# Kernel optimization log

Hardware: AMD Instinct MI355X
Metric: run time of the kernel (lower is better)

The kernel has to match this reference:

```python
import jax, jax.numpy as jnp
import numpy as np

B_SZ = 64
SEQ = 2048
IN_DIM = 16
D_MODEL = 128
D_INNER = 256   # expand(2) * d_model
D_STATE = 16
N_LAYERS = 5
N_PARAMS = 3
IDX_PRICE, IDX_RY, IDX_GY, IDX_NY = 0, 1, 2, 3


def setup_inputs() -> dict:
    key = jax.random.key(0)
    ks = iter(jax.random.split(key, 64))
    def nrm(shape, scale=0.02):
        return jax.random.normal(next(ks), shape, jnp.float32) * scale
    inp = {}
    # forward args
    inp["origins"] = jax.random.uniform(next(ks), (B_SZ, SEQ, IN_DIM), jnp.float32, 0.5, 1.5)
    inp["x"] = jax.random.normal(next(ks), (B_SZ, SEQ, IN_DIM), jnp.float32)
    # input embedding
    inp["emb_w"] = nrm((IN_DIM, D_MODEL)); inp["emb_b"] = jnp.zeros((D_MODEL,), jnp.float32)
    # per-layer Mamba block params, stacked on leading n_layers dim
    inp["in_w"] = nrm((N_LAYERS, D_MODEL, 2 * D_INNER)); inp["in_b"] = jnp.zeros((N_LAYERS, 2 * D_INNER), jnp.float32)
    inp["xp_w"] = nrm((N_LAYERS, D_INNER, 2 * D_STATE)); inp["xp_b"] = jnp.zeros((N_LAYERS, 2 * D_STATE), jnp.float32)
    inp["dt_w"] = nrm((N_LAYERS, D_INNER, D_INNER));     inp["dt_b"] = jnp.zeros((N_LAYERS, D_INNER), jnp.float32)
    inp["out_w"] = nrm((N_LAYERS, D_INNER, D_MODEL));    inp["out_b"] = jnp.zeros((N_LAYERS, D_MODEL), jnp.float32)
    # A_log init: log(arange(1, d_state+1)) broadcast over d_inner
    a = jnp.log(jnp.arange(1, D_STATE + 1, dtype=jnp.float32))
    inp["A_log"] = jnp.broadcast_to(a, (N_LAYERS, D_INNER, D_STATE)).copy()
    inp["Dp"] = jnp.ones((N_LAYERS, D_INNER), jnp.float32)
    # layernorms
    inp["ln_g"] = jnp.ones((N_LAYERS, D_MODEL), jnp.float32)
    inp["ln_b"] = jnp.zeros((N_LAYERS, D_MODEL), jnp.float32)
    # output head: Linear(128,64) -> ReLU -> Linear(64,3) -> Sigmoid
    inp["o1_w"] = nrm((D_MODEL, D_MODEL // 2)); inp["o1_b"] = jnp.zeros((D_MODEL // 2,), jnp.float32)
    inp["o2_w"] = nrm((D_MODEL // 2, N_PARAMS)); inp["o2_b"] = jnp.zeros((N_PARAMS,), jnp.float32)
    return inp


def _silu(x):
    return x * jax.nn.sigmoid(x)


def _layernorm(x, g, b, eps=1e-5):
    mu = jnp.mean(x, axis=-1, keepdims=True)
    var = jnp.mean(jnp.square(x - mu), axis=-1, keepdims=True)
    return (x - mu) * jax.lax.rsqrt(var + eps) * g + b


def _mamba_block(x, iw, ib, xw, xb, dw, db, ow, ob, alog, d):
    # x: [B, S, D_MODEL]
    xz = x @ iw + ib                       # [B,S,2*di]
    x_proj, z = jnp.split(xz, 2, axis=-1)  # [B,S,di] each
    u = _silu(x_proj)                      # no conv path (use_conv=False)
    A = -jnp.exp(alog)                     # [di, ds]
    x_dbl = u @ xw + xb                    # [B,S,2*ds]
    Bm, Cm = jnp.split(x_dbl, 2, axis=-1)  # [B,S,ds]
    dt = jax.nn.softplus(u @ dw + db)      # [B,S,di]

    def step(h, t):
        u_t, dt_t, B_t, C_t = t            # [B,di],[B,di],[B,ds],[B,ds]
        dA = jnp.exp(dt_t[:, :, None] * A)                 # [B,di,ds]
        h = h * dA + (dt_t * u_t)[:, :, None] * B_t[:, None, :]
        y = jnp.sum(h * C_t[:, None, :], axis=-1) + d * u_t  # [B,di]
        return h, y

    h0 = jnp.zeros((u.shape[0], u.shape[2], A.shape[-1]), u.dtype)
    xs = (jnp.swapaxes(u, 0, 1), jnp.swapaxes(dt, 0, 1),
          jnp.swapaxes(Bm, 0, 1), jnp.swapaxes(Cm, 0, 1))  # seq-major
    _, ys = jax.lax.scan(step, h0, xs)     # ys: [S,B,di]
    y = jnp.swapaxes(ys, 0, 1)             # [B,S,di]
    y = y * _silu(z)
    return y @ ow + ob                     # [B,S,D_MODEL]


def _forward(origins, x, emb_w, emb_b, in_w, in_b, xp_w, xp_b, dt_w, dt_b,
             out_w, out_b, A_log, Dp, ln_g, ln_b, o1_w, o1_b, o2_w, o2_b):
    h = x @ emb_w + emb_b
    for l in range(N_LAYERS):
        res = h
        h = _mamba_block(h, in_w[l], in_b[l], xp_w[l], xp_b[l], dt_w[l], dt_b[l],
                         out_w[l], out_b[l], A_log[l], Dp[l])
        h = _layernorm(h + res, ln_g[l], ln_b[l])
    pooled = jnp.mean(h, axis=1)                         # lengths=None path
    hid = jax.nn.relu(pooled @ o1_w + o1_b)              # dropout is eval no-op
    params = jax.nn.sigmoid(hid @ o2_w + o2_b) * 2.0     # [B, 3]
    a, b, c = params[:, 0], params[:, 1], params[:, 2]
    last_1 = origins[:, -1, :]
    last_2 = origins[:, -2, :]
    price = last_1[:, IDX_PRICE]
    ry_now, ry_before = last_1[:, IDX_RY], last_2[:, IDX_RY]
    gy_now, gy_before = last_1[:, IDX_GY], last_2[:, IDX_GY]
    ny_now, ny_before = last_1[:, IDX_NY], last_2[:, IDX_NY]
    out = price * a * ry_now / ry_before * 2.0 * (
        b * jax.nn.sigmoid(gy_now - gy_before) + c * jax.nn.sigmoid(ny_now - ny_before))
    return out  # [B]


def reference(origins, x, emb_w, emb_b, in_w, in_b, xp_w, xp_b, dt_w, dt_b,
              out_w, out_b, A_log, Dp, ln_g, ln_b, o1_w, o1_b, o2_w, o2_b):
    return _forward(origins, x, emb_w, emb_b, in_w, in_b, xp_w, xp_b, dt_w, dt_b,
                    out_w, out_b, A_log, Dp, ln_g, ln_b, o1_w, o1_b, o2_w, o2_b)
```

## Files before the change

### kernel.cpp

```cpp
#include <hip/hip_runtime.h>
#include <hip/hip_bf16.h>
#include <math.h>

#define B_SZ    64
#define SEQ     2048
#define DMODEL  128
#define DINNER  256
#define DSTATE  16
#define NLAYERS 5

typedef unsigned short u16;
typedef __attribute__((ext_vector_type(8))) short bf16x8;
typedef __attribute__((ext_vector_type(4))) float f32x4;

static __device__ __forceinline__ float bf2f(u16 u){
  union { unsigned u; float f; } a; a.u = ((unsigned)u) << 16; return a.f;
}
static __device__ __forceinline__ u16 f2bf(float f){
  union { float f; unsigned u; } a; a.f = f;
  unsigned r = a.u + 0x7fffu + ((a.u >> 16) & 1u);
  return (u16)(r >> 16);
}
static __device__ __forceinline__ float sigm(float x){ return 1.f/(1.f+__expf(-x)); }
static __device__ __forceinline__ float siluf(float x){ return x/(1.f+__expf(-x)); }

#define MFMA16(a,b,c) __builtin_amdgcn_mfma_f32_16x16x32_bf16((a),(b),(c),0,0,0)

__global__ __launch_bounds__(256) void prep_kernel(
    const float* __restrict__ in_w, const float* __restrict__ xp_w,
    const float* __restrict__ dt_w, const float* __restrict__ out_w,
    u16* __restrict__ WT1, u16* __restrict__ WT2, u16* __restrict__ WT3){
  int idx = blockIdx.x*256 + threadIdx.x;
  const int n1 = NLAYERS*512*128, n2 = NLAYERS*288*256, n3 = NLAYERS*128*256;
  if (idx < n1){
    int l = idx/(512*128), r = idx%(512*128), n = r/128, k = r%128;
    WT1[idx] = f2bf(in_w[((size_t)l*128 + k)*512 + n]);
  } else if (idx < n1+n2){
    int t = idx-n1; int l=t/(288*256), r=t%(288*256), n=r/256, k=r%256;
    float v = (n<32) ? xp_w[((size_t)l*256+k)*32 + n]
                     : dt_w[((size_t)l*256+k)*256 + (n-32)];
    WT2[t] = f2bf(v);
  } else if (idx < n1+n2+n3){
    int t = idx-n1-n2; int l=t/(128*256), r=t%(128*256), n=r/256, k=r%256;
    WT3[t] = f2bf(out_w[((size_t)l*256+k)*128 + n]);
  }
}

__global__ __launch_bounds__(256) void emb_kernel(
    const float* __restrict__ x, const float* __restrict__ ew,
    const float* __restrict__ eb, u16* __restrict__ Hb, size_t cs){
  int idx = blockIdx.x*256 + threadIdx.x;
  int m = idx >> 7, d = idx & 127;
  float s = eb[d];
  #pragma unroll
  for (int k=0;k<16;++k) s += x[(size_t)m*16+k]*ew[k*128+d];
  Hb[(size_t)(d>>4)*cs + (size_t)m*16 + (d&15)] = f2bf(s);
}

__global__ __launch_bounds__(256) void gemm1_kernel(
    const u16* __restrict__ Hb, const u16* __restrict__ WT,
    const float* __restrict__ bias, u16* __restrict__ U, u16* __restrict__ ZS,
    size_t cs){
  const int lane = threadIdx.x & 63, wave = threadIdx.x >> 6;
  const int half = blockIdx.x & 1;
  const int m0 = (blockIdx.x >> 1)*256 + wave*64;
  const int lr = lane & 15, kg = lane >> 4;
  bf16x8 hfrag[4][4];
  #pragma unroll
  for (int g=0; g<4; ++g)
    #pragma unroll
    for (int f=0; f<4; ++f)
      hfrag[g][f] = *(const bf16x8*)(Hb + (size_t)((kg>>1)+2*f)*cs
                                     + (size_t)(m0+g*16+lr)*16 + (kg&1)*8);
  u16* const dst = half ? ZS : U;
  const u16* wrow = WT + (size_t)(half*256+lr)*128 + kg*8;
  bf16x8 wv[4];
  #pragma unroll
  for (int f=0; f<4; ++f) wv[f] = *(const bf16x8*)(wrow + f*32);
  #pragma unroll
  for (int nn=0; nn<16; ++nn){
    bf16x8 wn[4];
    if (nn < 15){
      const u16* wr2 = wrow + (size_t)(nn+1)*16*128;
      #pragma unroll
      for (int f=0; f<4; ++f) wn[f] = *(const bf16x8*)(wr2 + f*32);
    }
    f32x4 acc[4];
    #pragma unroll
    for (int g=0; g<4; ++g){
      acc[g] = (f32x4){0.f,0.f,0.f,0.f};
      #pragma unroll
      for (int f=0; f<4; ++f) acc[g] = MFMA16(wv[f], hfrag[g][f], acc[g]);
    }
    float4 bs4 = *(const float4*)(bias + half*256 + nn*16 + kg*4);
    #pragma unroll
    for (int g=0; g<4; ++g){
      ushort4 uv;
      uv.x = f2bf(siluf(acc[g][0]+bs4.x));
      uv.y = f2bf(siluf(acc[g][1]+bs4.y));
      uv.z = f2bf(siluf(acc[g][2]+bs4.z));
      uv.w = f2bf(siluf(acc[g][3]+bs4.w));
      *(ushort4*)(dst + (size_t)nn*cs + (size_t)(m0+g*16+lr)*16 + kg*4) = uv;
    }
    #pragma unroll
    for (int f=0; f<4; ++f) wv[f] = wn[f];
  }
}

template<int BF>
__global__ __launch_bounds__(256) void gemm2_kernel(
    const u16* __restrict__ Uin, const u16* __restrict__ WT,
    const float* __restrict__ xpb, const float* __restrict__ dtb,
    void* __restrict__ BCv, u16* __restrict__ DT, size_t cs){
  const int lane = threadIdx.x & 63, wave = threadIdx.x >> 6;
  const int m0 = blockIdx.x*128 + wave*32;
  const int lr = lane & 15, kg = lane >> 4;
  bf16x8 hfrag[2][8];
  #pragma unroll
  for (int g=0; g<2; ++g)
    #pragma unroll
    for (int f=0; f<8; ++f)
      hfrag[g][f] = *(const bf16x8*)(Uin + (size_t)((kg>>1)+2*f)*cs
                                     + (size_t)(m0+g*16+lr)*16 + (kg&1)*8);
  const u16* wrow = WT + (size_t)lr*256 + kg*8;
  bf16x8 wv[8];
  #pragma unroll
  for (int f=0; f<8; ++f) wv[f] = *(const bf16x8*)(wrow + f*32);
  #pragma unroll
  for (int nn=0; nn<18; ++nn){
    bf16x8 wn[8];
    if (nn < 17){
      const u16* wr2 = wrow + (size_t)(nn+1)*16*256;
      #pragma unroll
      for (int f=0; f<8; ++f) wn[f] = *(const bf16x8*)(wr2 + f*32);
    }
    f32x4 acc[2];
    #pragma unroll
    for (int g=0; g<2; ++g){
      acc[g] = (f32x4){0.f,0.f,0.f,0.f};
      #pragma unroll
      for (int f=0; f<8; ++f) acc[g] = MFMA16(wv[f], hfrag[g][f], acc[g]);
    }
    const int col0 = nn*16 + kg*4;
    if (col0 < 32){
      float4 bs4 = *(const float4*)(xpb + col0);
      #pragma unroll
      for (int g=0; g<2; ++g){
        if (BF){
          float4 ov;
          ov.x = acc[g][0]+bs4.x; ov.y = acc[g][1]+bs4.y;
          ov.z = acc[g][2]+bs4.z; ov.w = acc[g][3]+bs4.w;
          *(float4*)((float*)BCv + (size_t)nn*cs + (size_t)(m0+g*16+lr)*16 + kg*4) = ov;
        } else {
          ushort4 uv;
          uv.x = f2bf(acc[g][0]+bs4.x); uv.y = f2bf(acc[g][1]+bs4.y);
          uv.z = f2bf(acc[g][2]+bs4.z); uv.w = f2bf(acc[g][3]+bs4.w);
          *(ushort4*)((u16*)BCv + (size_t)nn*cs + (size_t)(m0+g*16+lr)*16 + kg*4) = uv;
        }
      }
    } else {
      float4 bs4 = *(const float4*)(dtb + (col0-32));
      #pragma unroll
      for (int g=0; g<2; ++g){
        float v0=acc[g][0]+bs4.x, v1=acc[g][1]+bs4.y;
        float v2=acc[g][2]+bs4.z, v3=acc[g][3]+bs4.w;
        ushort4 uv;
        uv.x = f2bf(fmaxf(v0,0.f) + __logf(1.f + __expf(-fabsf(v0))));
        uv.y = f2bf(fmaxf(v1,0.f) + __logf(1.f + __expf(-fabsf(v1))));
        uv.z = f2bf(fmaxf(v2,0.f) + __logf(1.f + __expf(-fabsf(v2))));
        uv.w = f2bf(fmaxf(v3,0.f) + __logf(1.f + __expf(-fabsf(v3))));
        *(ushort4*)(DT + (size_t)(nn-2)*cs + (size_t)(m0+g*16+lr)*16 + kg*4) = uv;
      }
    }
    #pragma unroll
    for (int f=0; f<8; ++f) wv[f] = wn[f];
  }
}

static __device__ __forceinline__ void powtree(float r, float* pw){
  float p2=r*r, p3=p2*r, p4=p2*p2;
  float p5=p4*r, p6=p4*p2, p7=p4*p3, p8=p4*p4;
  pw[0]=r;  pw[1]=p2; pw[2]=p3; pw[3]=p4;
  pw[4]=p5; pw[5]=p6; pw[6]=p7; pw[7]=p8;
  pw[8]=p8*r;  pw[9]=p8*p2;  pw[10]=p8*p3;  pw[11]=p8*p4;
  pw[12]=p8*p5; pw[13]=p8*p6; pw[14]=p8*p7; pw[15]=p8*p8;
}


template<int BF>
__global__ __launch_bounds__(256) void scan_p1(
    const u16* __restrict__ U, const u16* __restrict__ DT,
    const void* __restrict__ BCv, const float* __restrict__ Alog,
    u16* __restrict__ SGH, size_t cs, int nseg, int L){
  const int seg = blockIdx.x % nseg;
  const int b   = blockIdx.x / nseg;
  const int c   = threadIdx.x;
  const size_t coff = (size_t)(c>>4)*cs + (c&15);
  float a2[16]; bool geo = true;
  #pragma unroll
  for (int i=0;i<16;++i){
    float A = -__expf(Alog[c*16+i]);
    a2[i] = A * 1.44269504f;
    if (fabsf(A + (float)(i+1)) > 1e-3f) geo = false;
  }
  float h[16];
  #pragma unroll
  for (int i=0;i<16;++i) h[i]=0.f;
  float sdt = 0.f;
  const size_t mbase = (size_t)b*SEQ + (size_t)seg*L;
  if (geo){
    #pragma unroll 2
    for (int t=0;t<L;++t){
      const size_t m = mbase + t;
      float u  = bf2f(U [coff + m*16]);
      float dt = bf2f(DT[coff + m*16]);
      float Bv[16];
      if (BF){
        const float* bp = (const float*)BCv + m*16;
        #pragma unroll
        for (int i=0;i<16;++i) Bv[i] = bp[i];
      } else {
        bf16x8 b0 = *(const bf16x8*)((const u16*)BCv + m*16);
        bf16x8 b1 = *(const bf16x8*)((const u16*)BCv + m*16 + 8);
        #pragma unroll
        for (int i=0;i<8;++i){ Bv[i]=bf2f((u16)b0[i]); Bv[i+8]=bf2f((u16)b1[i]); }
      }
      float du = dt*u; sdt += dt;
      float r = exp2f(-1.44269504f*dt);
      float pw[16]; powtree(r, pw);
      #pragma unroll
      for (int i=0;i<16;++i) h[i] = h[i]*pw[i] + du*Bv[i];
    }
  } else {
    for (int t=0;t<L;++t){
      const size_t m = mbase + t;
      float u  = bf2f(U [coff + m*16]);
      float dt = bf2f(DT[coff + m*16]);
      float Bv[16];
      if (BF){
        const float* bp = (const float*)BCv + m*16;
        #pragma unroll
        for (int i=0;i<16;++i) Bv[i] = bp[i];
      } else {
        bf16x8 b0 = *(const bf16x8*)((const u16*)BCv + m*16);
        bf16x8 b1 = *(const bf16x8*)((const u16*)BCv + m*16 + 8);
        #pragma unroll
        for (int i=0;i<8;++i){ Bv[i]=bf2f((u16)b0[i]); Bv[i+8]=bf2f((u16)b1[i]); }
      }
      float du = dt*u; sdt += dt;
      #pragma unroll
      for (int i=0;i<16;++i)
        h[i] = h[i]*exp2f(dt*a2[i]) + du*Bv[i];
    }
  }
  const size_t kb = ((size_t)b*nseg+seg);
  #pragma unroll
  for (int i=0;i<16;++i) SGH[(kb*17+i)*256 + c] = f2bf(h[i]);
  SGH[(kb*17+16)*256 + c] = f2bf(sdt);
}

__global__ __launch_bounds__(256) void scan_p2(
    u16* __restrict__ SGH, const float* __restrict__ Alog, int nseg){
  const int i = blockIdx.x & 15, b = blockIdx.x >> 4, c = threadIdx.x;
  const float a2 = -__expf(Alog[c*16+i]) * 1.44269504f;
  float h = 0.f;
  for (int s=0;s<nseg;++s){
    const size_t kb = ((size_t)b*nseg+s);
    float sdt = bf2f(SGH[(kb*17+16)*256 + c]);
    size_t k = (kb*17+i)*256 + c;
    float hl = bf2f(SGH[k]);
    SGH[k] = f2bf(h);
    h = h*exp2f(sdt*a2) + hl;
  }
}

template<int BF>
__global__ __launch_bounds__(256) void scan_p3(
    u16* __restrict__ UY, const u16* __restrict__ DT, const void* __restrict__ BCv,
    const u16* __restrict__ ZS, const float* __restrict__ Alog,
    const float* __restrict__ Dp, const u16* __restrict__ SGH, size_t cs,
    int nseg, int L){
  const int seg = blockIdx.x % nseg;
  const int b   = blockIdx.x / nseg;
  const int c   = threadIdx.x;
  const size_t coff = (size_t)(c>>4)*cs + (c&15);
  float a2[16]; bool geo = true;
  #pragma unroll
  for (int i=0;i<16;++i){
    float A = -__expf(Alog[c*16+i]);
    a2[i] = A * 1.44269504f;
    if (fabsf(A + (float)(i+1)) > 1e-3f) geo = false;
  }
  const float Dv = Dp[c];
  const size_t kb = ((size_t)b*nseg+seg);
  float h[16];
  #pragma unroll
  for (int i=0;i<16;++i) h[i] = bf2f(SGH[(kb*17+i)*256 + c]);
  const size_t mbase = (size_t)b*SEQ + (size_t)seg*L;
  if (geo){
    #pragma unroll 2
    for (int t=0;t<L;++t){
      const size_t m = mbase + t;
      float u  = bf2f(UY[coff + m*16]);
      float dt = bf2f(DT[coff + m*16]);
      float zs = bf2f(ZS[coff + m*16]);
      float Bv[16], Cv[16];
      if (BF){
        const float* bp = (const float*)BCv + m*16;
        const float* cp = (const float*)BCv + cs + m*16;
        #pragma unroll
        for (int i=0;i<16;++i){ Bv[i]=bp[i]; Cv[i]=cp[i]; }
      } else {
        const u16* bc = (const u16*)BCv;
        bf16x8 b0 = *(const bf16x8*)(bc + m*16);
        bf16x8 b1 = *(const bf16x8*)(bc + m*16 + 8);
        bf16x8 c0 = *(const bf16x8*)(bc + cs + m*16);
        bf16x8 c1 = *(const bf16x8*)(bc + cs + m*16 + 8);
        #pragma unroll
        for (int i=0;i<8;++i){
          Bv[i]=bf2f((u16)b0[i]); Bv[i+8]=bf2f((u16)b1[i]);
          Cv[i]=bf2f((u16)c0[i]); Cv[i+8]=bf2f((u16)c1[i]);
        }
      }
      float du = dt*u;
      float r = exp2f(-1.44269504f*dt);
      float pw[16]; powtree(r, pw);
      float s0=0.f, s1=0.f;
      #pragma unroll
      for (int i=0;i<8;++i){
        h[i] = h[i]*pw[i] + du*Bv[i];
        s0 += h[i]*Cv[i];
      }
      #pragma unroll
      for (int i=8;i<16;++i){
        h[i] = h[i]*pw[i] + du*Bv[i];
        s1 += h[i]*Cv[i];
      }
      float y = s0 + s1 + Dv*u;
      UY[coff + m*16] = f2bf(y*zs);
    }
  } else {
    for (int t=0;t<L;++t){
      const size_t m = mbase + t;
      float u  = bf2f(UY[coff + m*16]);
      float dt = bf2f(DT[coff + m*16]);
      float zs = bf2f(ZS[coff + m*16]);
      float Bv[16], Cv[16];
      if (BF){
        const float* bp = (const float*)BCv + m*16;
        const float* cp = (const float*)BCv + cs + m*16;
        #pragma unroll
        for (int i=0;i<16;++i){ Bv[i]=bp[i]; Cv[i]=cp[i]; }
      } else {
        const u16* bc = (const u16*)BCv;
        bf16x8 b0 = *(const bf16x8*)(bc + m*16);
        bf16x8 b1 = *(const bf16x8*)(bc + m*16 + 8);
        bf16x8 c0 = *(const bf16x8*)(bc + cs + m*16);
        bf16x8 c1 = *(const bf16x8*)(bc + cs + m*16 + 8);
        #pragma unroll
        for (int i=0;i<8;++i){
          Bv[i]=bf2f((u16)b0[i]); Bv[i+8]=bf2f((u16)b1[i]);
          Cv[i]=bf2f((u16)c0[i]); Cv[i+8]=bf2f((u16)c1[i]);
        }
      }
      float du = dt*u;
      float s0=0.f;
      #pragma unroll
      for (int i=0;i<16;++i){
        h[i] = h[i]*exp2f(dt*a2[i]) + du*Bv[i];
        s0 += h[i]*Cv[i];
      }
      float y = s0 + Dv*u;
      UY[coff + m*16] = f2bf(y*zs);
    }
  }
}

__global__ __launch_bounds__(256) void gemm3ln_kernel(
    const u16* __restrict__ YS, const u16* __restrict__ WT,
    const float* __restrict__ ob, const float* __restrict__ g,
    const float* __restrict__ bb, u16* __restrict__ Hb, size_t cs){
  const int lane = threadIdx.x & 63, wave = threadIdx.x >> 6;
  const int m0 = blockIdx.x*128 + wave*32;
  const int lr = lane & 15, kg = lane >> 4;
  bf16x8 hfrag[2][8];
  #pragma unroll
  for (int gg=0; gg<2; ++gg)
    #pragma unroll
    for (int f=0; f<8; ++f)
      hfrag[gg][f] = *(const bf16x8*)(YS + (size_t)((kg>>1)+2*f)*cs
                                      + (size_t)(m0+gg*16+lr)*16 + (kg&1)*8);
  const u16* wrow = WT + (size_t)lr*256 + kg*8;
  bf16x8 wv[8];
  #pragma unroll
  for (int f=0; f<8; ++f) wv[f] = *(const bf16x8*)(wrow + f*32);
  ushort4 xvp[2][8];
  float s[2] = {0.f,0.f}, q[2] = {0.f,0.f};
  #pragma unroll
  for (int n=0; n<8; ++n){
    bf16x8 wn[8];
    if (n < 7){
      const u16* wr2 = wrow + (size_t)(n+1)*16*256;
      #pragma unroll
      for (int f=0; f<8; ++f) wn[f] = *(const bf16x8*)(wr2 + f*32);
    }
    float4 bs4 = *(const float4*)(ob + n*16 + kg*4);
    #pragma unroll
    for (int gg=0; gg<2; ++gg){
      f32x4 acc = {0.f,0.f,0.f,0.f};
      #pragma unroll
      for (int f=0; f<8; ++f) acc = MFMA16(wv[f], hfrag[gg][f], acc);
      const size_t m = (size_t)(m0 + gg*16 + lr);
      ushort4 rs = *(const ushort4*)(Hb + (size_t)n*cs + m*16 + kg*4);
      float x0 = acc[0] + bs4.x + bf2f(rs.x);
      float x1 = acc[1] + bs4.y + bf2f(rs.y);
      float x2 = acc[2] + bs4.z + bf2f(rs.z);
      float x3 = acc[3] + bs4.w + bf2f(rs.w);
      s[gg] += (x0+x1)+(x2+x3);
      q[gg] += (x0*x0+x1*x1)+(x2*x2+x3*x3);
      ushort4 pv; pv.x=f2bf(x0); pv.y=f2bf(x1); pv.z=f2bf(x2); pv.w=f2bf(x3);
      xvp[gg][n] = pv;
    }
    #pragma unroll
    for (int f=0; f<8; ++f) wv[f] = wn[f];
  }
  #pragma unroll
  for (int gg=0; gg<2; ++gg){
    float ss = s[gg], qq = q[gg];
    ss += __shfl_xor(ss,16); qq += __shfl_xor(qq,16);
    ss += __shfl_xor(ss,32); qq += __shfl_xor(qq,32);
    float mu  = ss * 0.0078125f;
    float var = qq * 0.0078125f - mu*mu;
    float inv = rsqrtf(var + 1e-5f);
    const size_t m = (size_t)(m0 + gg*16 + lr);
    #pragma unroll
    for (int n=0;n<8;++n){
      float4 g4 = *(const float4*)(g  + n*16 + kg*4);
      float4 b4 = *(const float4*)(bb + n*16 + kg*4);
      ushort4 pv = xvp[gg][n];
      ushort4 uv;
      uv.x = f2bf((bf2f(pv.x)-mu)*inv*g4.x + b4.x);
      uv.y = f2bf((bf2f(pv.y)-mu)*inv*g4.y + b4.y);
      uv.z = f2bf((bf2f(pv.z)-mu)*inv*g4.z + b4.z);
      uv.w = f2bf((bf2f(pv.w)-mu)*inv*g4.w + b4.w);
      *(ushort4*)(Hb + (size_t)n*cs + m*16 + kg*4) = uv;
    }
  }
}

__global__ __launch_bounds__(128) void pool1_kernel(
    const u16* __restrict__ Hb, float* __restrict__ PP, size_t cs){
  const int blk = blockIdx.x;
  const int tc = blk & 15, b = blk >> 4;
  const int d = threadIdx.x;
  const size_t coff = (size_t)(d>>4)*cs + (d&15);
  float s = 0.f;
  const size_t base = ((size_t)b*SEQ + tc*128);
  for (int t=0;t<128;++t) s += bf2f(Hb[coff + (base+t)*16]);
  PP[((size_t)b*16 + tc)*128 + d] = s;
}
__global__ __launch_bounds__(128) void pool2_kernel(
    const float* __restrict__ PP, float* __restrict__ P){
  const int b = blockIdx.x, d = threadIdx.x;
  float s = 0.f;
  #pragma unroll
  for (int tc=0;tc<16;++tc) s += PP[((size_t)b*16+tc)*128 + d];
  P[b*128 + d] = s * (1.f/SEQ);
}

__global__ __launch_bounds__(64) void head_kernel(
    const float* __restrict__ P, const float* __restrict__ o1w,
    const float* __restrict__ o1b, const float* __restrict__ o2w,
    const float* __restrict__ o2b, const float* __restrict__ origins,
    float* __restrict__ out){
  const int b = blockIdx.x;
  const int j = threadIdx.x;
  float hv = o1b[j];
  #pragma unroll 4
  for (int d=0; d<128; ++d) hv += P[b*128+d]*o1w[d*64+j];
  hv = fmaxf(hv, 0.f);
  float p0 = hv*o2w[j*3+0], p1 = hv*o2w[j*3+1], p2 = hv*o2w[j*3+2];
  #pragma unroll
  for (int o=1;o<64;o<<=1){
    p0 += __shfl_xor(p0,o); p1 += __shfl_xor(p1,o); p2 += __shfl_xor(p2,o);
  }
  if (j == 0){
    float a = 2.f*sigm(p0 + o2b[0]);
    float bb = 2.f*sigm(p1 + o2b[1]);
    float c = 2.f*sigm(p2 + o2b[2]);
    const float* l1 = origins + ((size_t)b*SEQ + (SEQ-1))*16;
    const float* l2 = origins + ((size_t)b*SEQ + (SEQ-2))*16;
    float price=l1[0], ry_n=l1[1], ry_b=l2[1], gy_n=l1[2], gy_b=l2[2], ny_n=l1[3], ny_b=l2[3];
    out[b] = price*a*ry_n/ry_b*2.f*(bb*sigm(gy_n-gy_b) + c*sigm(ny_n-ny_b));
  }
}

extern "C" void kernel_launch(void* const* d_in, const int* in_sizes, int n_in,
                              void* d_out, int out_size, void* d_ws, size_t ws_size,
                              hipStream_t stream){
  const float* origins = (const float*)d_in[0];
  const float* x      = (const float*)d_in[1];
  const float* emb_w  = (const float*)d_in[2];
  const float* emb_b  = (const float*)d_in[3];
  const float* in_w   = (const float*)d_in[4];
  const float* in_b   = (const float*)d_in[5];
  const float* xp_w   = (const float*)d_in[6];
  const float* xp_b   = (const float*)d_in[7];
  const float* dt_w   = (const float*)d_in[8];
  const float* dt_b   = (const float*)d_in[9];
  const float* out_w  = (const float*)d_in[10];
  const float* out_b  = (const float*)d_in[11];
  const float* A_log  = (const float*)d_in[12];
  const float* Dp     = (const float*)d_in[13];
  const float* ln_g   = (const float*)d_in[14];
  const float* ln_b   = (const float*)d_in[15];
  const float* o1_w   = (const float*)d_in[16];
  const float* o1_b   = (const float*)d_in[17];
  const float* o2_w   = (const float*)d_in[18];
  const float* o2_b   = (const float*)d_in[19];
  float* outp = (float*)d_out;

  auto al = [](size_t b)->size_t{ return (b + 255) & ~(size_t)255; };
  const size_t wt1_b = al((size_t)NLAYERS*512*128*2);
  const size_t wt2_b = al((size_t)NLAYERS*288*256*2);
  const size_t wt3_b = al((size_t)NLAYERS*128*256*2);
  const size_t po_b  = al((size_t)B_SZ*128*4);
  const size_t pp_b  = al((size_t)B_SZ*16*128*4);
  const size_t fixed = wt1_b + wt2_b + wt3_b + po_b;

  int CB = 0, NSEG = 0, BCF = 0;
  size_t hb_b=0, u_b=0, bc_b=0, sg_b=0;
  static const int cbc[7]  = {64,32,16,8,4,2,1};
  static const int nsc[4]  = {32,16,32,16};
  static const int bfc[4]  = {1,1,0,0};
  for (int i=0;i<7 && !CB;++i){
    int cb = cbc[i];
    size_t csz = (size_t)cb*SEQ*16;
    for (int k=0;k<4;++k){
      int ns = nsc[k], bf = bfc[k];
      size_t hbb = al(8*csz*2);
      size_t uu  = al(16*csz*2);
      size_t bb  = al(2*csz*(bf?4:2));
      size_t sg  = al((size_t)cb*ns*17*256*2);
      size_t ov  = (sg > pp_b) ? sg : pp_b;
      if (fixed + hbb + 3*uu + bb + ov <= ws_size){
        CB=cb; NSEG=ns; BCF=bf; hb_b=hbb; u_b=uu; bc_b=bb; sg_b=ov; break;
      }
    }
  }
  if (!CB) return;

  char* ws = (char*)d_ws;
  size_t off = 0;
  auto take = [&](size_t bytes)->char*{ char* p = ws + off; off += bytes; return p; };
  u16*   WT1 = (u16*)take(wt1_b);
  u16*   WT2 = (u16*)take(wt2_b);
  u16*   WT3 = (u16*)take(wt3_b);
  float* PO  = (float*)take(po_b);
  u16*   Hb  = (u16*)take(hb_b);
  u16*   U   = (u16*)take(u_b);
  u16*   ZS  = (u16*)take(u_b);
  u16*   DT  = (u16*)take(u_b);
  void*  BC  = (void*)take(bc_b);
  u16*   SGH = (u16*)take(sg_b);
  float* PP  = (float*)SGH;

  prep_kernel<<<3360, 256, 0, stream>>>(in_w, xp_w, dt_w, out_w, WT1, WT2, WT3);

  const int NC = B_SZ / CB;
  const int Mc = CB * SEQ;
  const int L  = SEQ / NSEG;
  const size_t cs = (size_t)Mc*16;
  for (int ci=0; ci<NC; ++ci){
    const int b0 = ci * CB;
    const size_t R0 = (size_t)b0 * SEQ;
    emb_kernel<<<(Mc*DMODEL)/256, 256, 0, stream>>>(x + R0*16, emb_w, emb_b, Hb, cs);
    for (int l=0;l<NLAYERS;++l){
      const float* Al = A_log + (size_t)l*DINNER*DSTATE;
      gemm1_kernel<<<(Mc/256)*2, 256, 0, stream>>>(Hb, WT1 + (size_t)l*512*128,
                                                   in_b + l*512, U, ZS, cs);
      if (BCF)
        gemm2_kernel<1><<<Mc/128, 256, 0, stream>>>(U, WT2 + (size_t)l*288*256,
                                                    xp_b + l*32, dt_b + l*256, BC, DT, cs);
      else
        gemm2_kernel<0><<<Mc/128, 256, 0, stream>>>(U, WT2 + (size_t)l*288*256,
                                                    xp_b + l*32, dt_b + l*256, BC, DT, cs);
      if (BCF){
        scan_p1<1><<<CB*NSEG, 256, 0, stream>>>(U, DT, BC, Al, SGH, cs, NSEG, L);
        scan_p2<<<CB*16, 256, 0, stream>>>(SGH, Al, NSEG);
        scan_p3<1><<<CB*NSEG, 256, 0, stream>>>(U, DT, BC, ZS, Al, Dp + l*DINNER,
                                                SGH, cs, NSEG, L);
      } else {
        scan_p1<0><<<CB*NSEG, 256, 0, stream>>>(U, DT, BC, Al, SGH, cs, NSEG, L);
        scan_p2<<<CB*16, 256, 0, stream>>>(SGH, Al, NSEG);
        scan_p3<0><<<CB*NSEG, 256, 0, stream>>>(U, DT, BC, ZS, Al, Dp + l*DINNER,
                                                SGH, cs, NSEG, L);
      }
      gemm3ln_kernel<<<Mc/128, 256, 0, stream>>>(U, WT3 + (size_t)l*128*256,
                                                 out_b + l*128, ln_g + l*128,
                                                 ln_b + l*128, Hb, cs);
    }
    pool1_kernel<<<CB*16, 128, 0, stream>>>(Hb, PP, cs);
    pool2_kernel<<<CB, 128, 0, stream>>>(PP, PO + (size_t)b0*128);
  }
  head_kernel<<<B_SZ, 64, 0, stream>>>(PO, o1_w, o1_b, o2_w, o2_b, origins, outp);
}
```

Before: 1.832 ms.

## Process two channels per thread in scan kernels and store C always in bf16

The selective-scan kernels now give each thread two adjacent channels with 128-thread blocks. Paired U/DT/ZS loads and packed SGH/Y stores use 32-bit accesses, and each loaded B/C value feeds two recurrences. C moves to its own bf16 buffer while B keeps the selectable fp32/bf16 format, and the workspace search now prefers fp32 B with 32 segments. The aim is to cut per-channel load work and memory traffic in the scan, but it halves the thread count per segment and raises register pressure.

Result: slower. 1.990 ms (+8.6%).

```diff
diff --git a/kernel.cpp b/kernel.cpp
--- a/kernel.cpp
+++ b/kernel.cpp
@@ -10,6 +10,7 @@
 #define NLAYERS 5
 
 typedef unsigned short u16;
+typedef unsigned int   u32;
 typedef __attribute__((ext_vector_type(8))) short bf16x8;
 typedef __attribute__((ext_vector_type(4))) float f32x4;
 
@@ -111,7 +112,8 @@
 __global__ __launch_bounds__(256) void gemm2_kernel(
     const u16* __restrict__ Uin, const u16* __restrict__ WT,
     const float* __restrict__ xpb, const float* __restrict__ dtb,
-    void* __restrict__ BCv, u16* __restrict__ DT, size_t cs){
+    void* __restrict__ Bp, u16* __restrict__ Cb, u16* __restrict__ DT,
+    size_t cs){
   const int lane = threadIdx.x & 63, wave = threadIdx.x >> 6;
   const int m0 = blockIdx.x*128 + wave*32;
   const int lr = lane & 15, kg = lane >> 4;
@@ -142,7 +144,7 @@
       for (int f=0; f<8; ++f) acc[g] = MFMA16(wv[f], hfrag[g][f], acc[g]);
     }
     const int col0 = nn*16 + kg*4;
-    if (col0 < 32){
+    if (nn == 0){
       float4 bs4 = *(const float4*)(xpb + col0);
       #pragma unroll
       for (int g=0; g<2; ++g){
@@ -150,13 +152,22 @@
           float4 ov;
           ov.x = acc[g][0]+bs4.x; ov.y = acc[g][1]+bs4.y;
           ov.z = acc[g][2]+bs4.z; ov.w = acc[g][3]+bs4.w;
-          *(float4*)((float*)BCv + (size_t)nn*cs + (size_t)(m0+g*16+lr)*16 + kg*4) = ov;
+          *(float4*)((float*)Bp + (size_t)(m0+g*16+lr)*16 + kg*4) = ov;
         } else {
           ushort4 uv;
           uv.x = f2bf(acc[g][0]+bs4.x); uv.y = f2bf(acc[g][1]+bs4.y);
           uv.z = f2bf(acc[g][2]+bs4.z); uv.w = f2bf(acc[g][3]+bs4.w);
-          *(ushort4*)((u16*)BCv + (size_t)nn*cs + (size_t)(m0+g*16+lr)*16 + kg*4) = uv;
+          *(ushort4*)((u16*)Bp + (size_t)(m0+g*16+lr)*16 + kg*4) = uv;
         }
+      }
+    } else if (nn == 1){
+      float4 bs4 = *(const float4*)(xpb + col0);
+      #pragma unroll
+      for (int g=0; g<2; ++g){
+        ushort4 uv;
+        uv.x = f2bf(acc[g][0]+bs4.x); uv.y = f2bf(acc[g][1]+bs4.y);
+        uv.z = f2bf(acc[g][2]+bs4.z); uv.w = f2bf(acc[g][3]+bs4.w);
+        *(ushort4*)(Cb + (size_t)(m0+g*16+lr)*16 + (col0-16)) = uv;
       }
     } else {
       float4 bs4 = *(const float4*)(dtb + (col0-32));
@@ -186,77 +197,102 @@
   pw[12]=p8*p5; pw[13]=p8*p6; pw[14]=p8*p7; pw[15]=p8*p8;
 }
 
+static __device__ __forceinline__ bool geo_check(const float* Alog, int c0, int c1){
+  bool geo = true;
+  #pragma unroll
+  for (int i=0;i<16;++i){
+    float A0 = -__expf(Alog[c0*16+i]);
+    float A1 = -__expf(Alog[c1*16+i]);
+    if (fabsf(A0+(float)(i+1))>1e-3f || fabsf(A1+(float)(i+1))>1e-3f) geo = false;
+  }
+  return geo;
+}
+
 
 template<int BF>
-__global__ __launch_bounds__(256) void scan_p1(
+__global__ __launch_bounds__(128) void scan_p1(
     const u16* __restrict__ U, const u16* __restrict__ DT,
-    const void* __restrict__ BCv, const float* __restrict__ Alog,
+    const void* __restrict__ Bp, const float* __restrict__ Alog,
     u16* __restrict__ SGH, size_t cs, int nseg, int L){
   const int seg = blockIdx.x % nseg;
   const int b   = blockIdx.x / nseg;
-  const int c   = threadIdx.x;
-  const size_t coff = (size_t)(c>>4)*cs + (c&15);
-  float a2[16]; bool geo = true;
-  #pragma unroll
-  for (int i=0;i<16;++i){
-    float A = -__expf(Alog[c*16+i]);
-    a2[i] = A * 1.44269504f;
-    if (fabsf(A + (float)(i+1)) > 1e-3f) geo = false;
-  }
-  float h[16];
-  #pragma unroll
-  for (int i=0;i<16;++i) h[i]=0.f;
-  float sdt = 0.f;
+  const int t   = threadIdx.x;
+  const int c0  = 2*t, c1 = 2*t+1;
+  const size_t poff = (size_t)(c0>>4)*cs + (c0&15);
+  const bool geo = geo_check(Alog, c0, c1);
+  float h0[16], h1[16];
+  #pragma unroll
+  for (int i=0;i<16;++i){ h0[i]=0.f; h1[i]=0.f; }
+  float sdt0 = 0.f, sdt1 = 0.f;
   const size_t mbase = (size_t)b*SEQ + (size_t)seg*L;
   if (geo){
-    #pragma unroll 2
-    for (int t=0;t<L;++t){
-      const size_t m = mbase + t;
-      float u  = bf2f(U [coff + m*16]);
-      float dt = bf2f(DT[coff + m*16]);
+    for (int tt=0;tt<L;++tt){
+      const size_t m = mbase + tt;
+      u32 uu = *(const u32*)(U  + poff + m*16);
+      u32 dd = *(const u32*)(DT + poff + m*16);
+      float u0 = bf2f((u16)uu), u1 = bf2f((u16)(uu>>16));
+      float d0 = bf2f((u16)dd), d1 = bf2f((u16)(dd>>16));
       float Bv[16];
       if (BF){
-        const float* bp = (const float*)BCv + m*16;
+        const float* bp = (const float*)Bp + m*16;
         #pragma unroll
         for (int i=0;i<16;++i) Bv[i] = bp[i];
       } else {
-        bf16x8 b0 = *(const bf16x8*)((const u16*)BCv + m*16);
-        bf16x8 b1 = *(const bf16x8*)((const u16*)BCv + m*16 + 8);
-        #pragma unroll
-        for (int i=0;i<8;++i){ Bv[i]=bf2f((u16)b0[i]); Bv[i+8]=bf2f((u16)b1[i]); }
-      }
-      float du = dt*u; sdt += dt;
-      float r = exp2f(-1.44269504f*dt);
-      float pw[16]; powtree(r, pw);
-      #pragma unroll
-      for (int i=0;i<16;++i) h[i] = h[i]*pw[i] + du*Bv[i];
+        const u16* bp = (const u16*)Bp + m*16;
+        #pragma unroll
+        for (int i=0;i<16;++i) Bv[i] = bf2f(bp[i]);
+      }
+      float du0 = d0*u0, du1 = d1*u1;
+      sdt0 += d0; sdt1 += d1;
+      float r0 = exp2f(-1.44269504f*d0);
+      float r1 = exp2f(-1.44269504f*d1);
+      float pw0[16], pw1[16]; powtree(r0, pw0); powtree(r1, pw1);
+      #pragma unroll
+      for (int i=0;i<16;++i){
+        h0[i] = h0[i]*pw0[i] + du0*Bv[i];
+        h1[i] = h1[i]*pw1[i] + du1*Bv[i];
+      }
     }
   } else {
-    for (int t=0;t<L;++t){
-      const size_t m = mbase + t;
-      float u  = bf2f(U [coff + m*16]);
-      float dt = bf2f(DT[coff + m*16]);
+    float a20[16], a21[16];
+    #pragma unroll
+    for (int i=0;i<16;++i){
+      a20[i] = -__expf(Alog[c0*16+i]) * 1.44269504f;
+      a21[i] = -__expf(Alog[c1*16+i]) * 1.44269504f;
+    }
+    for (int tt=0;tt<L;++tt){
+      const size_t m = mbase + tt;
+      u32 uu = *(const u32*)(U  + poff + m*16);
+      u32 dd = *(const u32*)(DT + poff + m*16);
+      float u0 = bf2f((u16)uu), u1 = bf2f((u16)(uu>>16));
+      float d0 = bf2f((u16)dd), d1 = bf2f((u16)(dd>>16));
       float Bv[16];
       if (BF){
-        const float* bp = (const float*)BCv + m*16;
+        const float* bp = (const float*)Bp + m*16;
         #pragma unroll
         for (int i=0;i<16;++i) Bv[i] = bp[i];
       } else {
-        bf16x8 b0 = *(const bf16x8*)((const u16*)BCv + m*16);
-        bf16x8 b1 = *(const bf16x8*)((const u16*)BCv + m*16 + 8);
-        #pragma unroll
-        for (int i=0;i<8;++i){ Bv[i]=bf2f((u16)b0[i]); Bv[i+8]=bf2f((u16)b1[i]); }
-      }
-      float du = dt*u; sdt += dt;
-      #pragma unroll
-      for (int i=0;i<16;++i)
-        h[i] = h[i]*exp2f(dt*a2[i]) + du*Bv[i];
+        const u16* bp = (const u16*)Bp + m*16;
+        #pragma unroll
+        for (int i=0;i<16;++i) Bv[i] = bf2f(bp[i]);
+      }
+      float du0 = d0*u0, du1 = d1*u1;
+      sdt0 += d0; sdt1 += d1;
+      #pragma unroll
+      for (int i=0;i<16;++i){
+        h0[i] = h0[i]*exp2f(d0*a20[i]) + du0*Bv[i];
+        h1[i] = h1[i]*exp2f(d1*a21[i]) + du1*Bv[i];
+      }
     }
   }
   const size_t kb = ((size_t)b*nseg+seg);
   #pragma unroll
-  for (int i=0;i<16;++i) SGH[(kb*17+i)*256 + c] = f2bf(h[i]);
-  SGH[(kb*17+16)*256 + c] = f2bf(sdt);
+  for (int i=0;i<16;++i){
+    u32 pk = (u32)f2bf(h0[i]) | ((u32)f2bf(h1[i]) << 16);
+    *(u32*)(SGH + (kb*17+i)*256 + c0) = pk;
+  }
+  u32 ps = (u32)f2bf(sdt0) | ((u32)f2bf(sdt1) << 16);
+  *(u32*)(SGH + (kb*17+16)*256 + c0) = ps;
 }
 
 __global__ __launch_bounds__(256) void scan_p2(
@@ -275,103 +311,110 @@
 }
 
 template<int BF>
-__global__ __launch_bounds__(256) void scan_p3(
-    u16* __restrict__ UY, const u16* __restrict__ DT, const void* __restrict__ BCv,
-    const u16* __restrict__ ZS, const float* __restrict__ Alog,
-    const float* __restrict__ Dp, const u16* __restrict__ SGH, size_t cs,
-    int nseg, int L){
+__global__ __launch_bounds__(128) void scan_p3(
+    u16* __restrict__ UY, const u16* __restrict__ DT, const void* __restrict__ Bp,
+    const u16* __restrict__ Cb, const u16* __restrict__ ZS,
+    const float* __restrict__ Alog, const float* __restrict__ Dp,
+    const u16* __restrict__ SGH, size_t cs, int nseg, int L){
   const int seg = blockIdx.x % nseg;
   const int b   = blockIdx.x / nseg;
-  const int c   = threadIdx.x;
-  const size_t coff = (size_t)(c>>4)*cs + (c&15);
-  float a2[16]; bool geo = true;
+  const int t   = threadIdx.x;
+  const int c0  = 2*t, c1 = 2*t+1;
+  const size_t poff = (size_t)(c0>>4)*cs + (c0&15);
+  const bool geo = geo_check(Alog, c0, c1);
+  const float Dv0 = Dp[c0], Dv1 = Dp[c1];
+  const size_t kb = ((size_t)b*nseg+seg);
+  float h0[16], h1[16];
   #pragma unroll
   for (int i=0;i<16;++i){
-    float A = -__expf(Alog[c*16+i]);
-    a2[i] = A * 1.44269504f;
-    if (fabsf(A + (float)(i+1)) > 1e-3f) geo = false;
-  }
-  const float Dv = Dp[c];
-  const size_t kb = ((size_t)b*nseg+seg);
-  float h[16];
-  #pragma unroll
-  for (int i=0;i<16;++i) h[i] = bf2f(SGH[(kb*17+i)*256 + c]);
+    u32 hh = *(const u32*)(SGH + (kb*17+i)*256 + c0);
+    h0[i] = bf2f((u16)hh); h1[i] = bf2f((u16)(hh>>16));
+  }
   const size_t mbase = (size_t)b*SEQ + (size_t)seg*L;
   if (geo){
-    #pragma unroll 2
-    for (int t=0;t<L;++t){
-      const size_t m = mbase + t;
-      float u  = bf2f(UY[coff + m*16]);
-      float dt = bf2f(DT[coff + m*16]);
-      float zs = bf2f(ZS[coff + m*16]);
+    for (int tt=0;tt<L;++tt){
+      const size_t m = mbase + tt;
+      u32 uu = *(const u32*)(UY + poff + m*16);
+      u32 dd = *(const u32*)(DT + poff + m*16);
+      u32 zz = *(const u32*)(ZS + poff + m*16);
+      float u0 = bf2f((u16)uu), u1 = bf2f((u16)(uu>>16));
+      float d0 = bf2f((u16)dd), d1 = bf2f((u16)(dd>>16));
+      float z0 = bf2f((u16)zz), z1 = bf2f((u16)(zz>>16));
       float Bv[16], Cv[16];
       if (BF){
-        const float* bp = (const float*)BCv + m*16;
-        const float* cp = (const float*)BCv + cs + m*16;
-        #pragma unroll
-        for (int i=0;i<16;++i){ Bv[i]=bp[i]; Cv[i]=cp[i]; }
+        const float* bp = (const float*)Bp + m*16;
+        #pragma unroll
+        for (int i=0;i<16;++i) Bv[i] = bp[i];
       } else {
-        const u16* bc = (const u16*)BCv;
-        bf16x8 b0 = *(const bf16x8*)(bc + m*16);
-        bf16x8 b1 = *(const bf16x8*)(bc + m*16 + 8);
-        bf16x8 c0 = *(const bf16x8*)(bc + cs + m*16);
-        bf16x8 c1 = *(const bf16x8*)(bc + cs + m*16 + 8);
-        #pragma unroll
-        for (int i=0;i<8;++i){
-          Bv[i]=bf2f((u16)b0[i]); Bv[i+8]=bf2f((u16)b1[i]);
-          Cv[i]=bf2f((u16)c0[i]); Cv[i+8]=bf2f((u16)c1[i]);
-        }
-      }
-      float du = dt*u;
-      float r = exp2f(-1.44269504f*dt);
-      float pw[16]; powtree(r, pw);
-      float s0=0.f, s1=0.f;
-      #pragma unroll
-      for (int i=0;i<8;++i){
-        h[i] = h[i]*pw[i] + du*Bv[i];
-        s0 += h[i]*Cv[i];
-      }
-      #pragma unroll
-      for (int i=8;i<16;++i){
-        h[i] = h[i]*pw[i] + du*Bv[i];
-        s1 += h[i]*Cv[i];
-      }
-      float y = s0 + s1 + Dv*u;
-      UY[coff + m*16] = f2bf(y*zs);
+        const u16* bp = (const u16*)Bp + m*16;
+        #pragma unroll
+        for (int i=0;i<16;++i) Bv[i] = bf2f(bp[i]);
+      }
+      {
+        const u16* cp = Cb + m*16;
+        #pragma unroll
+        for (int i=0;i<16;++i) Cv[i] = bf2f(cp[i]);
+      }
+      float du0 = d0*u0, du1 = d1*u1;
+      float r0 = exp2f(-1.44269504f*d0);
+      float r1 = exp2f(-1.44269504f*d1);
+      float pw0[16], pw1[16]; powtree(r0, pw0); powtree(r1, pw1);
+      float s0 = 0.f, s1 = 0.f;
+      #pragma unroll
+      for (int i=0;i<16;++i){
+        h0[i] = h0[i]*pw0[i] + du0*Bv[i];
+        s0 += h0[i]*Cv[i];
+        h1[i] = h1[i]*pw1[i] + du1*Bv[i];
+        s1 += h1[i]*Cv[i];
+      }
+      float y0 = (s0 + Dv0*u0)*z0;
+      float y1 = (s1 + Dv1*u1)*z1;
+      u32 pk = (u32)f2bf(y0) | ((u32)f2bf(y1) << 16);
+      *(u32*)(UY + poff + m*16) = pk;
     }
   } else {
-    for (int t=0;t<L;++t){
-      const size_t m = mbase + t;
-      float u  = bf2f(UY[coff + m*16]);
-      float dt = bf2f(DT[coff + m*16]);
-      float zs = bf2f(ZS[coff + m*16]);
+    float a20[16], a21[16];
+    #pragma unroll
+    for (int i=0;i<16;++i){
+      a20[i] = -__expf(Alog[c0*16+i]) * 1.44269504f;
+      a21[i] = -__expf(Alog[c1*16+i]) * 1.44269504f;
+    }
+    for (int tt=0;tt<L;++tt){
+      const size_t m = mbase + tt;
+      u32 uu = *(const u32*)(UY + poff + m*16);
+      u32 dd = *(const u32*)(DT + poff + m*16);
+      u32 zz = *(const u32*)(ZS + poff + m*16);
+      float u0 = bf2f((u16)uu), u1 = bf2f((u16)(uu>>16));
+      float d0 = bf2f((u16)dd), d1 = bf2f((u16)(dd>>16));
+      float z0 = bf2f((u16)zz), z1 = bf2f((u16)(zz>>16));
       float Bv[16], Cv[16];
       if (BF){
-        const float* bp = (const float*)BCv + m*16;
-        const float* cp = (const float*)BCv + cs + m*16;
-        #pragma unroll
-        for (int i=0;i<16;++i){ Bv[i]=bp[i]; Cv[i]=cp[i]; }
+        const float* bp = (const float*)Bp + m*16;
+        #pragma unroll
+        for (int i=0;i<16;++i) Bv[i] = bp[i];
       } else {
-        const u16* bc = (const u16*)BCv;
-        bf16x8 b0 = *(const bf16x8*)(bc + m*16);
-        bf16x8 b1 = *(const bf16x8*)(bc + m*16 + 8);
-        bf16x8 c0 = *(const bf16x8*)(bc + cs + m*16);
-        bf16x8 c1 = *(const bf16x8*)(bc + cs + m*16 + 8);
-        #pragma unroll
-        for (int i=0;i<8;++i){
-          Bv[i]=bf2f((u16)b0[i]); Bv[i+8]=bf2f((u16)b1[i]);
-          Cv[i]=bf2f((u16)c0[i]); Cv[i+8]=bf2f((u16)c1[i]);
-        }
-      }
-      float du = dt*u;
-      float s0=0.f;
+        const u16* bp = (const u16*)Bp + m*16;
+        #pragma unroll
+        for (int i=0;i<16;++i) Bv[i] = bf2f(bp[i]);
+      }
+      {
+        const u16* cp = Cb + m*16;
+        #pragma unroll
+        for (int i=0;i<16;++i) Cv[i] = bf2f(cp[i]);
+      }
+      float du0 = d0*u0, du1 = d1*u1;
+      float s0 = 0.f, s1 = 0.f;
       #pragma unroll
       for (int i=0;i<16;++i){
-        h[i] = h[i]*exp2f(dt*a2[i]) + du*Bv[i];
-        s0 += h[i]*Cv[i];
-      }
-      float y = s0 + Dv*u;
-      UY[coff + m*16] = f2bf(y*zs);
+        h0[i] = h0[i]*exp2f(d0*a20[i]) + du0*Bv[i];
+        s0 += h0[i]*Cv[i];
+        h1[i] = h1[i]*exp2f(d1*a21[i]) + du1*Bv[i];
+        s1 += h1[i]*Cv[i];
+      }
+      float y0 = (s0 + Dv0*u0)*z0;
+      float y1 = (s1 + Dv1*u1)*z1;
+      u32 pk = (u32)f2bf(y0) | ((u32)f2bf(y1) << 16);
+      *(u32*)(UY + poff + m*16) = pk;
     }
   }
 }
@@ -529,10 +572,10 @@
   const size_t fixed = wt1_b + wt2_b + wt3_b + po_b;
 
   int CB = 0, NSEG = 0, BCF = 0;
-  size_t hb_b=0, u_b=0, bc_b=0, sg_b=0;
+  size_t hb_b=0, u_b=0, b_b=0, c_b=0, sg_b=0;
   static const int cbc[7]  = {64,32,16,8,4,2,1};
-  static const int nsc[4]  = {32,16,32,16};
-  static const int bfc[4]  = {1,1,0,0};
+  static const int nsc[4]  = {32,32,16,16};
+  static const int bfc[4]  = {1,0,1,0};
   for (int i=0;i<7 && !CB;++i){
     int cb = cbc[i];
     size_t csz = (size_t)cb*SEQ*16;
@@ -540,11 +583,12 @@
       int ns = nsc[k], bf = bfc[k];
       size_t hbb = al(8*csz*2);
       size_t uu  = al(16*csz*2);
-      size_t bb  = al(2*csz*(bf?4:2));
+      size_t bB  = al(csz*(bf?4:2));
+      size_t bC  = al(csz*2);
       size_t sg  = al((size_t)cb*ns*17*256*2);
       size_t ov  = (sg > pp_b) ? sg : pp_b;
-      if (fixed + hbb + 3*uu + bb + ov <= ws_size){
-        CB=cb; NSEG=ns; BCF=bf; hb_b=hbb; u_b=uu; bc_b=bb; sg_b=ov; break;
+      if (fixed + hbb + 3*uu + bB + bC + ov <= ws_size){
+        CB=cb; NSEG=ns; BCF=bf; hb_b=hbb; u_b=uu; b_b=bB; c_b=bC; sg_b=ov; break;
       }
     }
   }
@@ -561,7 +605,8 @@
   u16*   U   = (u16*)take(u_b);
   u16*   ZS  = (u16*)take(u_b);
   u16*   DT  = (u16*)take(u_b);
-  void*  BC  = (void*)take(bc_b);
+  void*  Bp  = (void*)take(b_b);
+  u16*   Cb  = (u16*)take(c_b);
   u16*   SGH = (u16*)take(sg_b);
   float* PP  = (float*)SGH;
 
@@ -579,22 +624,22 @@
       const float* Al = A_log + (size_t)l*DINNER*DSTATE;
       gemm1_kernel<<<(Mc/256)*2, 256, 0, stream>>>(Hb, WT1 + (size_t)l*512*128,
                                                    in_b + l*512, U, ZS, cs);
-      if (BCF)
+      if (BCF){
         gemm2_kernel<1><<<Mc/128, 256, 0, stream>>>(U, WT2 + (size_t)l*288*256,
-                                                    xp_b + l*32, dt_b + l*256, BC, DT, cs);
-      else
+                                                    xp_b + l*32, dt_b + l*256,
+                                                    Bp, Cb, DT, cs);
+        scan_p1<1><<<CB*NSEG, 128, 0, stream>>>(U, DT, Bp, Al, SGH, cs, NSEG, L);
+        scan_p2<<<CB*16, 256, 0, stream>>>(SGH, Al, NSEG);
+        scan_p3<1><<<CB*NSEG, 128, 0, stream>>>(U, DT, Bp, Cb, ZS, Al,
+                                                Dp + l*DINNER, SGH, cs, NSEG, L);
+      } else {
         gemm2_kernel<0><<<Mc/128, 256, 0, stream>>>(U, WT2 + (size_t)l*288*256,
-                                                    xp_b + l*32, dt_b + l*256, BC, DT, cs);
-      if (BCF){
-        scan_p1<1><<<CB*NSEG, 256, 0, stream>>>(U, DT, BC, Al, SGH, cs, NSEG, L);
+                                                    xp_b + l*32, dt_b + l*256,
+                                                    Bp, Cb, DT, cs);
+        scan_p1<0><<<CB*NSEG, 128, 0, stream>>>(U, DT, Bp, Al, SGH, cs, NSEG, L);
         scan_p2<<<CB*16, 256, 0, stream>>>(SGH, Al, NSEG);
-        scan_p3<1><<<CB*NSEG, 256, 0, stream>>>(U, DT, BC, ZS, Al, Dp + l*DINNER,
-                                                SGH, cs, NSEG, L);
-      } else {
-        scan_p1<0><<<CB*NSEG, 256, 0, stream>>>(U, DT, BC, Al, SGH, cs, NSEG, L);
-        scan_p2<<<CB*16, 256, 0, stream>>>(SGH, Al, NSEG);
-        scan_p3<0><<<CB*NSEG, 256, 0, stream>>>(U, DT, BC, ZS, Al, Dp + l*DINNER,
-                                                SGH, cs, NSEG, L);
+        scan_p3<0><<<CB*NSEG, 128, 0, stream>>>(U, DT, Bp, Cb, ZS, Al,
+                                                Dp + l*DINNER, SGH, cs, NSEG, L);
       }
       gemm3ln_kernel<<<Mc/128, 256, 0, stream>>>(U, WT3 + (size_t)l*128*256,
                                                  out_b + l*128, ln_g + l*128,
```
